# Kernel optimization log

Measured on AMD Instinct MI355X. Metric: run time of the kernel, lower is better.

## Reference

```python
import jax, jax.numpy as jnp
import numpy as np

B, S, E, H, D = 2, 2048, 512, 8, 64
NEG = -1e10


def setup_inputs() -> dict:
    key = jax.random.key(0)
    k1, k2, k3, k4, k5, k6 = jax.random.split(key, 6)
    inputs = jax.random.normal(k1, (B, S, E), dtype=jnp.float32)
    keys = jax.random.normal(k2, (B, S, H, D), dtype=jnp.float32)
    values = jax.random.normal(k3, (B, S, H, D), dtype=jnp.float32)
    # xavier-uniform style scale for square weights
    lim = float(np.sqrt(6.0 / (E + H * D)))
    query_weights = jax.random.uniform(k4, (E, H * D), minval=-lim, maxval=lim, dtype=jnp.float32)
    output_weights = jax.random.uniform(k5, (H * D, E), minval=-lim, maxval=lim, dtype=jnp.float32)
    mask = jax.random.randint(k6, (B, S, S), 0, 2).astype(jnp.bool_)
    return {"inputs": inputs, "keys": keys, "values": values,
            "query_weights": query_weights, "output_weights": output_weights,
            "mask": mask}


def reference(inputs, keys, values, query_weights, output_weights, mask):
    # project queries: (B,S,E) @ (E,H*D) -> (B,S,H,D)
    q = jnp.matmul(inputs, query_weights).reshape(B, S, H, D)
    # scores: (B,H,Sq,Sk)
    scores = jnp.einsum('bqhd,bkhd->bhqk', q, keys) / jnp.sqrt(jnp.float32(D))
    # masked_fill(mask, -1e10); mask broadcasts over heads
    scores = jnp.where(mask[:, None, :, :], jnp.float32(NEG), scores)
    probs = jax.nn.softmax(scores, axis=-1)
    # (B,H,Sq,Sk) x (B,Sk,H,D) -> (B,Sq,H,D)
    out = jnp.einsum('bhqk,bkhd->bqhd', probs, values)
    out = out.reshape(B, S, H * D)
    return jnp.matmul(out, output_weights)
```

## Files before the change

kernel.cpp:

```cpp
#include <hip/hip_runtime.h>
#include <hip/hip_bf16.h>

namespace {

constexpr int B = 2, S = 2048, E = 512, H = 8, D = 64, HD = 512;
constexpr float SL = 0.125f * 1.44269504f;
constexpr int PLD = 40;

typedef __attribute__((ext_vector_type(8))) short bf16x8;
typedef __attribute__((ext_vector_type(4))) unsigned short u16x4;
typedef __attribute__((ext_vector_type(4))) float f32x4;
typedef __attribute__((ext_vector_type(4))) float float4v;

__device__ __forceinline__ ushort f2b(float x) {
  __hip_bfloat16 h = __float2bfloat16(x);
  return *reinterpret_cast<const ushort*>(&h);
}

__global__ __launch_bounds__(256) void prep_fused_kernel(
    const float* __restrict__ K, const float* __restrict__ V,
    const float* __restrict__ Wq, const float* __restrict__ Wo,
    const int* __restrict__ maskp,
    ushort* __restrict__ Kbf, ushort* __restrict__ Vtbf,
    ushort* __restrict__ Wtq, ushort* __restrict__ Wto,
    uint4* __restrict__ keep4) {
  const int bid = blockIdx.x;
  const int t = threadIdx.x;
  if (bid < 512) {
    __shared__ __align__(16) ushort Vn[64][76];
    const int kt = bid & 31;
    const int bh = bid >> 5;
    const int b = bh >> 3, h = bh & 7;
    const int k0 = kt * 64;
#pragma unroll
    for (int i = 0; i < 4; ++i) {
      int c = i * 256 + t;
      int kk = c >> 4, d4 = (c & 15) * 4;
      size_t g = ((size_t)(b * 2048 + k0 + kk) * 8 + h) * 64 + d4;
      float4v kv = *(const float4v*)(K + g);
      float4v vv = *(const float4v*)(V + g);
      u16x4 kp = {f2b(kv.x), f2b(kv.y), f2b(kv.z), f2b(kv.w)};
      u16x4 vp = {f2b(vv.x), f2b(vv.y), f2b(vv.z), f2b(vv.w)};
      *(u16x4*)(Kbf + ((size_t)(bh * 2048 + k0 + kk)) * 64 + d4) = kp;
      *(u16x4*)&Vn[kk][d4] = vp;
    }
    __syncthreads();
#pragma unroll
    for (int i = 0; i < 2; ++i) {
      int c = i * 256 + t;
      int kc8 = (c & 7) * 8, d = c >> 3;
      union { ushort u[8]; bf16x8 v; } p;
#pragma unroll
      for (int j = 0; j < 8; ++j) p.u[j] = Vn[kc8 + j][d];
      *(bf16x8*)(Vtbf + ((size_t)(bh * 64 + d)) * 2048 + k0 + kc8) = p.v;
    }
  } else if (bid < 640) {
    __shared__ __align__(16) ushort T[64][68];
    const int idx = bid - 512;
    const float* Wsrc = (idx >> 6) ? Wo : Wq;
    ushort* Wdst = (idx >> 6) ? Wto : Wtq;
    const int x = idx & 63;
    const int k0 = (x & 7) * 64, n0 = (x >> 3) * 64;
#pragma unroll
    for (int i = 0; i < 4; ++i) {
      int c = i * 256 + t;
      int kk = c >> 4, n4 = (c & 15) * 4;
      float4v v = *(const float4v*)(Wsrc + (size_t)(k0 + kk) * 512 + n0 + n4);
      u16x4 p = {f2b(v.x), f2b(v.y), f2b(v.z), f2b(v.w)};
      *(u16x4*)&T[kk][n4] = p;
    }
    __syncthreads();
#pragma unroll
    for (int i = 0; i < 2; ++i) {
      int c = i * 256 + t;
      int n = c >> 3, k8 = (c & 7) * 8;
      union { ushort u[8]; bf16x8 v; } p;
#pragma unroll
      for (int j = 0; j < 8; ++j) p.u[j] = T[k8 + j][n];
      *(bf16x8*)(Wdst + (size_t)(n0 + n) * 512 + k0 + k8) = p.v;
    }
  } else {
    const int wid = (bid - 640) * 4 + (t >> 6);
    const int row = wid >> 3, c = wid & 7;
    const int lane = t & 63;
    const int4 v = *((const int4*)(maskp + (size_t)row * 2048 + c * 256) + lane);
    unsigned long long bx = __ballot(v.x == 0);
    unsigned long long by = __ballot(v.y == 0);
    unsigned long long bz = __ballot(v.z == 0);
    unsigned long long bw = __ballot(v.w == 0);
    if (lane == 0)
      keep4[(size_t)row * 16 + c * 2] = uint4{(uint)bx, (uint)by, (uint)bz, (uint)bw};
    if (lane == 32)
      keep4[(size_t)row * 16 + c * 2 + 1] =
          uint4{(uint)(bx >> 32), (uint)(by >> 32), (uint)(bz >> 32), (uint)(bw >> 32)};
  }
}

__global__ __launch_bounds__(256) void proj_out_kernel(
    const ushort* __restrict__ A, const ushort* __restrict__ Wt, float* __restrict__ C) {
  __shared__ __align__(16) ushort As[64][PLD];
  __shared__ __align__(16) ushort Ws[64][PLD];

  const int tid = threadIdx.x;
  const int lane = tid & 63;
  const int w = tid >> 6;
  const int col = lane & 15;
  const int quad = lane >> 4;
  const int m0 = blockIdx.y * 64;
  const int n0 = blockIdx.x * 64;
  const int wm = (w & 1) * 32;
  const int wn = (w >> 1) * 32;
  const int ar = tid >> 2;
  const int ak = (tid & 3) * 8;
  const int wn2 = tid >> 2;
  const int wkc = (tid & 3) * 8;

  f32x4 acc[2][2];
#pragma unroll
  for (int i = 0; i < 2; ++i)
#pragma unroll
    for (int j = 0; j < 2; ++j) acc[i][j] = f32x4{0.f, 0.f, 0.f, 0.f};

  const ushort* Ap = A + (size_t)(m0 + ar) * 512 + ak;
  const ushort* Wp = Wt + (size_t)(n0 + wn2) * 512 + wkc;
  bf16x8 apre = *(const bf16x8*)Ap;
  bf16x8 wp = *(const bf16x8*)Wp;

  for (int kt = 0; kt < 16; ++kt) {
    if (kt) __syncthreads();
    *(bf16x8*)&As[ar][ak] = apre;
    *(bf16x8*)&Ws[wn2][wkc] = wp;
    if (kt < 15) {
      const int k1 = (kt + 1) * 32;
      apre = *(const bf16x8*)(Ap + k1);
      wp = *(const bf16x8*)(Wp + k1);
    }
    __syncthreads();

    bf16x8 ah[2], wb[2];
#pragma unroll
    for (int i = 0; i < 2; ++i)
      ah[i] = *(const bf16x8*)&As[wm + i * 16 + col][quad * 8];
#pragma unroll
    for (int j = 0; j < 2; ++j)
      wb[j] = *(const bf16x8*)&Ws[wn + j * 16 + col][quad * 8];
#pragma unroll
    for (int i = 0; i < 2; ++i)
#pragma unroll
      for (int j = 0; j < 2; ++j)
        acc[i][j] = __builtin_amdgcn_mfma_f32_16x16x32_bf16(ah[i], wb[j], acc[i][j], 0, 0, 0);
  }

#pragma unroll
  for (int i = 0; i < 2; ++i)
#pragma unroll
    for (int j = 0; j < 2; ++j)
#pragma unroll
      for (int r = 0; r < 4; ++r)
        C[(size_t)(m0 + wm + i * 16 + (quad << 2) + r) * 512 + n0 + wn + j * 16 + col] =
            acc[i][j][r];
}

__global__ __launch_bounds__(256, 2) void flash_attn_kernel(
    const float* __restrict__ inp, const ushort* __restrict__ Wtq,
    const ushort* __restrict__ Kbf, const ushort* __restrict__ Vtbf,
    const uint4* __restrict__ keep4, ushort* __restrict__ Op) {
  __shared__ __align__(16) union SM {
    struct { ushort Ks[128][72]; ushort Vt[64][136]; } m;
    ushort PQ[64][72];
    struct { float red[3][64][68]; float lred[3][64]; } r;
  } sm;

  const int bid = blockIdx.x;
  const int qt = bid & 31;
  const int bh = bid >> 5;
  const int b = bh >> 3, h = bh & 7;
  const int q0 = qt * 64;
  const int tid = threadIdx.x, lane = tid & 63, w = tid >> 6;
  const int col = lane & 15, quad = lane >> 4, quad4 = quad * 4;

  {
    f32x4 qacc[4];
#pragma unroll
    for (int n = 0; n < 4; ++n) qacc[n] = f32x4{0.f, 0.f, 0.f, 0.f};
    const float* Ap = inp + (size_t)(b * 2048 + q0 + w * 16 + col) * 512 + quad * 8;
    const ushort* Wp = Wtq + (size_t)(h * 64 + col) * 512 + quad * 8;
#pragma unroll 2
    for (int kk = 0; kk < 16; ++kk) {
      float4v a0 = *(const float4v*)(Ap + kk * 32);
      float4v a1 = *(const float4v*)(Ap + kk * 32 + 4);
      union { ushort u[8]; bf16x8 v; } ap;
      ap.u[0] = f2b(a0.x); ap.u[1] = f2b(a0.y); ap.u[2] = f2b(a0.z); ap.u[3] = f2b(a0.w);
      ap.u[4] = f2b(a1.x); ap.u[5] = f2b(a1.y); ap.u[6] = f2b(a1.z); ap.u[7] = f2b(a1.w);
#pragma unroll
      for (int n = 0; n < 4; ++n) {
        bf16x8 wb = *(const bf16x8*)(Wp + (size_t)(n * 16) * 512 + kk * 32);
        qacc[n] = __builtin_amdgcn_mfma_f32_16x16x32_bf16(ap.v, wb, qacc[n], 0, 0, 0);
      }
    }
#pragma unroll
    for (int n = 0; n < 4; ++n)
#pragma unroll
      for (int r = 0; r < 4; ++r)
        sm.PQ[w * 16 + quad4 + r][n * 16 + col] = f2b(qacc[n][r] * SL);
  }
  __syncthreads();

  bf16x8 qb[4][2];
#pragma unroll
  for (int j = 0; j < 4; ++j)
#pragma unroll
    for (int hf = 0; hf < 2; ++hf)
      qb[j][hf] = *(const bf16x8*)&sm.PQ[j * 16 + col][hf * 32 + quad * 8];
  __syncthreads();

  f32x4 oacc[4][4];
#pragma unroll
  for (int j = 0; j < 4; ++j)
#pragma unroll
    for (int c = 0; c < 4; ++c) oacc[j][c] = f32x4{0.f, 0.f, 0.f, 0.f};
  f32x4 lacc[4];
#pragma unroll
  for (int j = 0; j < 4; ++j) lacc[j] = f32x4{0.f, 0.f, 0.f, 0.f};

  union { ushort u[8]; bf16x8 v; } onesu;
#pragma unroll
  for (int j = 0; j < 8; ++j) onesu.u[j] = 0x3F80;
  const bf16x8 onesB = onesu.v;

  const uint4* kr0 = keep4 + (size_t)(b * 2048 + q0 + col) * 16;
  const ushort* Kbase = Kbf + (size_t)bh * 131072;
  const ushort* Vbase = Vtbf + (size_t)bh * 131072;
  const int mshift = 8 * w + quad;

  bf16x8 kpre[4], vpre[4];
#pragma unroll
  for (int i = 0; i < 4; ++i) {
    int c = i * 256 + tid;
    kpre[i] = *(const bf16x8*)(Kbase + (size_t)c * 8);
    int d = c >> 4, k8 = (c & 15) * 8;
    vpre[i] = *(const bf16x8*)(Vbase + (size_t)d * 2048 + k8);
  }

  for (int kt = 0; kt < 16; ++kt) {
    if (kt) __syncthreads();
#pragma unroll
    for (int i = 0; i < 4; ++i) {
      int c = i * 256 + tid;
      *(bf16x8*)&sm.m.Ks[c >> 3][(c & 7) * 8] = kpre[i];
      int d = c >> 4, k8 = (c & 15) * 8;
      *(bf16x8*)&sm.m.Vt[d][k8] = vpre[i];
    }
    uint4 kwj[4];
#pragma unroll
    for (int j = 0; j < 4; ++j) kwj[j] = kr0[j * 256 + kt];
    if (kt < 15) {
      const int k1 = (kt + 1) * 128;
#pragma unroll
      for (int i = 0; i < 4; ++i) {
        int c = i * 256 + tid;
        kpre[i] = *(const bf16x8*)(Kbase + (size_t)k1 * 64 + c * 8);
        int d = c >> 4, k8 = (c & 15) * 8;
        vpre[i] = *(const bf16x8*)(Vbase + (size_t)d * 2048 + k1 + k8);
      }
    }
    __syncthreads();

    bf16x8 ka[2][2];
#pragma unroll
    for (int t = 0; t < 2; ++t)
#pragma unroll
      for (int hf = 0; hf < 2; ++hf)
        ka[t][hf] = *(const bf16x8*)&sm.m.Ks[w * 32 + t * 16 + col][hf * 32 + quad * 8];

    f32x4 sc[2][4];
#pragma unroll
    for (int t = 0; t < 2; ++t)
#pragma unroll
      for (int j = 0; j < 4; ++j) sc[t][j] = f32x4{0.f, 0.f, 0.f, 0.f};
    __builtin_amdgcn_s_setprio(1);
#pragma unroll
    for (int t = 0; t < 2; ++t)
#pragma unroll
      for (int hf = 0; hf < 2; ++hf)
#pragma unroll
        for (int j = 0; j < 4; ++j)
          sc[t][j] = __builtin_amdgcn_mfma_f32_16x16x32_bf16(ka[t][hf], qb[j][hf], sc[t][j], 0, 0, 0);
    __builtin_amdgcn_s_setprio(0);

    bf16x8 vb[4];
#pragma unroll
    for (int c = 0; c < 4; ++c)
      vb[c] = *(const bf16x8*)&sm.m.Vt[c * 16 + col][w * 32 + quad * 8];

#pragma unroll
    for (int j = 0; j < 4; ++j) {
      const uint mx_ = kwj[j].x >> mshift, my_ = kwj[j].y >> mshift,
                 mz_ = kwj[j].z >> mshift, mw_ = kwj[j].w >> mshift;
      uint Xa0, Xa1, Xb0, Xb1;
      {
        float p0 = (mx_ & 1u) ? exp2f(sc[0][j][0]) : 0.f;
        float p1 = (my_ & 1u) ? exp2f(sc[0][j][1]) : 0.f;
        float p2 = (mz_ & 1u) ? exp2f(sc[0][j][2]) : 0.f;
        float p3 = (mw_ & 1u) ? exp2f(sc[0][j][3]) : 0.f;
        __hip_bfloat162 lo = __float22bfloat162_rn(float2{p0, p1});
        __hip_bfloat162 hi = __float22bfloat162_rn(float2{p2, p3});
        Xa0 = *reinterpret_cast<uint*>(&lo);
        Xa1 = *reinterpret_cast<uint*>(&hi);
      }
      {
        float p0 = ((mx_ >> 4) & 1u) ? exp2f(sc[1][j][0]) : 0.f;
        float p1 = ((my_ >> 4) & 1u) ? exp2f(sc[1][j][1]) : 0.f;
        float p2 = ((mz_ >> 4) & 1u) ? exp2f(sc[1][j][2]) : 0.f;
        float p3 = ((mw_ >> 4) & 1u) ? exp2f(sc[1][j][3]) : 0.f;
        __hip_bfloat162 lo = __float22bfloat162_rn(float2{p0, p1});
        __hip_bfloat162 hi = __float22bfloat162_rn(float2{p2, p3});
        Xb0 = *reinterpret_cast<uint*>(&lo);
        Xb1 = *reinterpret_cast<uint*>(&hi);
      }
      auto a32 = __builtin_amdgcn_permlane32_swap(Xa0, Xb0, false, false);
      auto a16 = __builtin_amdgcn_permlane16_swap(a32[0], a32[1], false, false);
      auto b32 = __builtin_amdgcn_permlane32_swap(Xa1, Xb1, false, false);
      auto b16 = __builtin_amdgcn_permlane16_swap(b32[0], b32[1], false, false);
      union { uint u[4]; bf16x8 v; } pu;
      pu.u[0] = a16[0]; pu.u[1] = b16[0]; pu.u[2] = a16[1]; pu.u[3] = b16[1];
      const bf16x8 pa = pu.v;
      __builtin_amdgcn_s_setprio(1);
      lacc[j] = __builtin_amdgcn_mfma_f32_16x16x32_bf16(pa, onesB, lacc[j], 0, 0, 0);
#pragma unroll
      for (int c = 0; c < 4; ++c)
        oacc[j][c] = __builtin_amdgcn_mfma_f32_16x16x32_bf16(pa, vb[c], oacc[j][c], 0, 0, 0);
      __builtin_amdgcn_s_setprio(0);
    }
  }

  __syncthreads();
  if (w > 0) {
    const int wi = w - 1;
#pragma unroll
    for (int j = 0; j < 4; ++j)
#pragma unroll
      for (int c = 0; c < 4; ++c)
        *(f32x4*)&sm.r.red[wi][c * 16 + col][j * 16 + quad4] = oacc[j][c];
    if (col == 0)
#pragma unroll
      for (int j = 0; j < 4; ++j)
        *(f32x4*)&sm.r.lred[wi][j * 16 + quad4] = lacc[j];
  }
  __syncthreads();
  if (w == 0) {
#pragma unroll
    for (int j = 0; j < 4; ++j) {
#pragma unroll
      for (int c = 0; c < 4; ++c) {
        f32x4 s = oacc[j][c];
#pragma unroll
        for (int i = 0; i < 3; ++i)
          s += *(const f32x4*)&sm.r.red[i][c * 16 + col][j * 16 + quad4];
        oacc[j][c] = s;
      }
      f32x4 ls = lacc[j];
#pragma unroll
      for (int i = 0; i < 3; ++i)
        ls += *(const f32x4*)&sm.r.lred[i][j * 16 + quad4];
      lacc[j] = ls;
    }
#pragma unroll
    for (int j = 0; j < 4; ++j) {
#pragma unroll
      for (int c = 0; c < 4; ++c)
        *(f32x4*)&sm.r.red[0][c * 16 + col][j * 16 + quad4] = oacc[j][c];
      if (col == 0) *(f32x4*)&sm.r.lred[0][j * 16 + quad4] = lacc[j];
    }
  }
  __syncthreads();

  {
    const int q = tid >> 2, d0 = (tid & 3) * 16;
    const float inv = 1.f / sm.r.lred[0][q];
    union { ushort u[16]; bf16x8 v[2]; } ob;
#pragma unroll
    for (int dd = 0; dd < 16; ++dd)
      ob.u[dd] = f2b(sm.r.red[0][d0 + dd][q] * inv);
    ushort* dst = Op + (size_t)(b * S + q0 + q) * HD + h * D + d0;
    *(bf16x8*)dst = ob.v[0];
    *(bf16x8*)(dst + 8) = ob.v[1];
  }
}

}

extern "C" void kernel_launch(void* const* d_in, const int* in_sizes, int n_in,
                              void* d_out, int out_size, void* d_ws, size_t ws_size,
                              hipStream_t stream) {
  const float* inputs = (const float*)d_in[0];
  const float* keys   = (const float*)d_in[1];
  const float* values = (const float*)d_in[2];
  const float* wq     = (const float*)d_in[3];
  const float* wo     = (const float*)d_in[4];
  const int*   maskp  = (const int*)d_in[5];
  float* out = (float*)d_out;

  ushort* Kbf  = (ushort*)d_out;
  ushort* Vtbf = Kbf + (size_t)2097152;

  char* ws = (char*)d_ws;
  ushort* attnb = (ushort*)ws;
  uint4*  keep4 = (uint4*)(ws + (4 << 20));
  ushort* Wtq   = (ushort*)(ws + (5 << 20));
  ushort* Wto   = (ushort*)(ws + (5 << 20) + (512 << 10));

  prep_fused_kernel<<<dim3(8832), dim3(256), 0, stream>>>(keys, values, wq, wo, maskp,
                                                          Kbf, Vtbf, Wtq, Wto, keep4);
  flash_attn_kernel<<<dim3(512), dim3(256), 0, stream>>>(inputs, Wtq, Kbf, Vtbf, keep4, attnb);
  proj_out_kernel<<<dim3(8, 64), dim3(256), 0, stream>>>(attnb, Wto, out);
}
```

Baseline: 170.2 us.

## Stage Q-projection operands through double-buffered LDS tiles with 2x2 warp tiling

Rewrites the fused Q-projection prologue of the flash-attention kernel. Input rows and Wq columns are now loaded cooperatively with coalesced 128-element chunks, converted to bf16 and staged into double-buffered shared memory. Each warp then computes a 32x32 output tile from LDS, so every warp no longer re-reads the full Wq slice from global memory. The cost is a larger shared-memory union, which may reduce occupancy, plus extra LDS traffic and barriers.

```diff
diff --git a/kernel.cpp b/kernel.cpp
--- a/kernel.cpp
+++ b/kernel.cpp
@@ -166,8 +166,9 @@
     const ushort* __restrict__ Kbf, const ushort* __restrict__ Vtbf,
     const uint4* __restrict__ keep4, ushort* __restrict__ Op) {
   __shared__ __align__(16) union SM {
+    struct { ushort A[2][64][136]; ushort W[2][64][136]; } p;
+    ushort PQ[64][72];
     struct { ushort Ks[128][72]; ushort Vt[64][136]; } m;
-    ushort PQ[64][72];
     struct { float red[3][64][68]; float lred[3][64]; } r;
   } sm;
 
@@ -178,33 +179,84 @@
   const int q0 = qt * 64;
   const int tid = threadIdx.x, lane = tid & 63, w = tid >> 6;
   const int col = lane & 15, quad = lane >> 4, quad4 = quad * 4;
+  const int wm = (w & 1) * 32;
+  const int wn = (w >> 1) * 32;
 
   {
-    f32x4 qacc[4];
-#pragma unroll
-    for (int n = 0; n < 4; ++n) qacc[n] = f32x4{0.f, 0.f, 0.f, 0.f};
-    const float* Ap = inp + (size_t)(b * 2048 + q0 + w * 16 + col) * 512 + quad * 8;
-    const ushort* Wp = Wtq + (size_t)(h * 64 + col) * 512 + quad * 8;
-#pragma unroll 2
-    for (int kk = 0; kk < 16; ++kk) {
-      float4v a0 = *(const float4v*)(Ap + kk * 32);
-      float4v a1 = *(const float4v*)(Ap + kk * 32 + 4);
-      union { ushort u[8]; bf16x8 v; } ap;
-      ap.u[0] = f2b(a0.x); ap.u[1] = f2b(a0.y); ap.u[2] = f2b(a0.z); ap.u[3] = f2b(a0.w);
-      ap.u[4] = f2b(a1.x); ap.u[5] = f2b(a1.y); ap.u[6] = f2b(a1.z); ap.u[7] = f2b(a1.w);
-#pragma unroll
-      for (int n = 0; n < 4; ++n) {
-        bf16x8 wb = *(const bf16x8*)(Wp + (size_t)(n * 16) * 512 + kk * 32);
-        qacc[n] = __builtin_amdgcn_mfma_f32_16x16x32_bf16(ap.v, wb, qacc[n], 0, 0, 0);
-      }
-    }
-#pragma unroll
-    for (int n = 0; n < 4; ++n)
-#pragma unroll
-      for (int r = 0; r < 4; ++r)
-        sm.PQ[w * 16 + quad4 + r][n * 16 + col] = f2b(qacc[n][r] * SL);
-  }
-  __syncthreads();
+    const int ar = tid >> 2;
+    const int ac = (tid & 3) * 32;
+
+    const float* Ap = inp + (size_t)(b * 2048 + q0 + ar) * 512 + ac;
+    const ushort* Wp = Wtq + (size_t)(h * 64 + ar) * 512 + ac;
+
+    float4v a[8];
+    bf16x8 wv[4];
+#define LOADP(KB)                                                          \
+  do {                                                                     \
+    _Pragma("unroll") for (int i_ = 0; i_ < 8; ++i_)                       \
+        a[i_] = *(const float4v*)(Ap + (KB) * 128 + i_ * 4);               \
+    _Pragma("unroll") for (int i_ = 0; i_ < 4; ++i_)                       \
+        wv[i_] = *(const bf16x8*)(Wp + (KB) * 128 + i_ * 8);               \
+  } while (0)
+#define STAGEP(BUF)                                                        \
+  do {                                                                     \
+    _Pragma("unroll") for (int i_ = 0; i_ < 4; ++i_) {                     \
+      union { ushort u[8]; bf16x8 v; } ap_;                                \
+      float4v lo_ = a[2 * i_], hi_ = a[2 * i_ + 1];                        \
+      ap_.u[0] = f2b(lo_.x); ap_.u[1] = f2b(lo_.y);                        \
+      ap_.u[2] = f2b(lo_.z); ap_.u[3] = f2b(lo_.w);                        \
+      ap_.u[4] = f2b(hi_.x); ap_.u[5] = f2b(hi_.y);                        \
+      ap_.u[6] = f2b(hi_.z); ap_.u[7] = f2b(hi_.w);                        \
+      *(bf16x8*)&sm.p.A[BUF][ar][ac + i_ * 8] = ap_.v;                     \
+      *(bf16x8*)&sm.p.W[BUF][ar][ac + i_ * 8] = wv[i_];                    \
+    }                                                                      \
+  } while (0)
+
+    f32x4 qacc[2][2];
+#pragma unroll
+    for (int i = 0; i < 2; ++i)
+#pragma unroll
+      for (int j = 0; j < 2; ++j) qacc[i][j] = f32x4{0.f, 0.f, 0.f, 0.f};
+
+    LOADP(0);
+    STAGEP(0);
+    LOADP(1);
+    __syncthreads();
+#pragma unroll 1
+    for (int kb = 0; kb < 4; ++kb) {
+      if (kb < 3) {
+        STAGEP((kb + 1) & 1);
+        if (kb < 2) LOADP(kb + 2);
+      }
+#pragma unroll
+      for (int ks = 0; ks < 4; ++ks) {
+        bf16x8 ah[2], wb[2];
+#pragma unroll
+        for (int i = 0; i < 2; ++i)
+          ah[i] = *(const bf16x8*)&sm.p.A[kb & 1][wm + i * 16 + col][ks * 32 + quad * 8];
+#pragma unroll
+        for (int j = 0; j < 2; ++j)
+          wb[j] = *(const bf16x8*)&sm.p.W[kb & 1][wn + j * 16 + col][ks * 32 + quad * 8];
+#pragma unroll
+        for (int i = 0; i < 2; ++i)
+#pragma unroll
+          for (int j = 0; j < 2; ++j)
+            qacc[i][j] = __builtin_amdgcn_mfma_f32_16x16x32_bf16(ah[i], wb[j], qacc[i][j], 0, 0, 0);
+      }
+      __syncthreads();
+    }
+#undef LOADP
+#undef STAGEP
+
+#pragma unroll
+    for (int i = 0; i < 2; ++i)
+#pragma unroll
+      for (int j = 0; j < 2; ++j)
+#pragma unroll
+        for (int r = 0; r < 4; ++r)
+          sm.PQ[wm + i * 16 + quad4 + r][wn + j * 16 + col] = f2b(qacc[i][j][r] * SL);
+    __syncthreads();
+  }
 
   bf16x8 qb[4][2];
 #pragma unroll
```

Result: faster. 161.4 us (-5.2%).
